# Kernel tuning notes

Measured on AMD Instinct MI355X. Metric: run time of the kernel, lower is better.

Reference implementation:

```python
import jax, jax.numpy as jnp
import numpy as np

N_NODES, N_EDGES, N_FEAT = 50000, 500000, 128
HID, LAT, N_GRAPHS = 256, 64, 512
HEADS, DH = 8, 32  # GAT: 8 heads x 32 = 256
EPS = 1e-5


def _seg_softmax(logits, seg, num):
    m = jax.ops.segment_max(logits, seg, num_segments=num)
    m = jnp.where(jnp.isfinite(m), m, 0.0)
    e = jnp.exp(logits - m[seg])
    s = jax.ops.segment_sum(e, seg, num_segments=num)
    return e / jnp.maximum(s[seg], 1e-16)


def _bn(h, g, b):  # BatchNorm1d, batch statistics
    mu = h.mean(0)
    var = h.var(0)
    return (h - mu) * jax.lax.rsqrt(var + EPS) * g + b


def _ln(h, g, b):
    mu = h.mean(-1, keepdims=True)
    var = h.var(-1, keepdims=True)
    return (h - mu) * jax.lax.rsqrt(var + EPS) * g + b


def setup_inputs() -> dict:
    key = jax.random.key(0)
    ks = iter(jax.random.split(key, 40))
    f = lambda *s: jax.random.normal(next(ks), s, dtype=jnp.float32) * 0.05
    inp = {
        'x': jax.random.normal(next(ks), (N_NODES, N_FEAT), dtype=jnp.float32),
        'W_emb': f(N_FEAT, HID), 'b_emb': f(HID),
        'W_gcn': f(HID, HID), 'b_gcn': f(HID),
        'W_gat': f(HID, HID), 'a_src': f(HEADS, DH), 'a_dst': f(HEADS, DH), 'b_gat': f(HID),
        'W_l': f(HID, HID), 'b_l': f(HID), 'W_r': f(HID, HID),
        'bn_gamma': jnp.ones((3, HID), jnp.float32), 'bn_beta': jnp.zeros((3, HID), jnp.float32),
        'Wg1': f(HID, HID // 2), 'bg1': f(HID // 2), 'Wg2': f(HID // 2, 1), 'bg2': f(1),
        'Wm1': f(HID, HID), 'bm1': f(HID), 'ln_m_g': jnp.ones(HID, jnp.float32), 'ln_m_b': jnp.zeros(HID, jnp.float32),
        'Wm2': f(HID, LAT), 'bm2': f(LAT),
        'Wv1': f(HID, HID), 'bv1': f(HID), 'ln_v_g': jnp.ones(HID, jnp.float32), 'ln_v_b': jnp.zeros(HID, jnp.float32),
        'Wv2': f(HID, LAT), 'bv2': f(LAT),
        'edge_index': jax.random.randint(next(ks), (2, N_EDGES), 0, N_NODES, dtype=jnp.int64),
        'batch': jnp.sort(jax.random.randint(next(ks), (N_NODES,), 0, N_GRAPHS, dtype=jnp.int64)),
    }
    return inp


def _forward(x, W_emb, b_emb, W_gcn, b_gcn, W_gat, a_src, a_dst, b_gat,
             W_l, b_l, W_r, bn_gamma, bn_beta, Wg1, bg1, Wg2, bg2,
             Wm1, bm1, ln_m_g, ln_m_b, Wm2, bm2, Wv1, bv1, ln_v_g, ln_v_b, Wv2, bv2,
             edge_index, batch):
    N = x.shape[0]
    loops = jnp.arange(N)
    src_sl = jnp.concatenate([edge_index[0], loops])  # with self-loops (GCN/GAT)
    dst_sl = jnp.concatenate([edge_index[1], loops])

    h = x @ W_emb + b_emb  # [N, HID]

    # --- layer 0: GCNConv ---
    deg = jax.ops.segment_sum(jnp.ones_like(dst_sl, dtype=h.dtype), dst_sl, num_segments=N)
    dis = jax.lax.rsqrt(deg)
    norm = dis[src_sl] * dis[dst_sl]  # [E+N]
    xt = h @ W_gcn
    out = jax.ops.segment_sum(xt[src_sl] * norm[:, None], dst_sl, num_segments=N) + b_gcn
    out = jax.nn.relu(_bn(out, bn_gamma[0], bn_beta[0]))
    h = h + out

    # --- layer 1: GATConv (8 heads, concat) ---
    xt = (h @ W_gat).reshape(N, HEADS, DH)
    al_src = (xt * a_src).sum(-1)  # [N, H]
    al_dst = (xt * a_dst).sum(-1)
    logits = jax.nn.leaky_relu(al_src[src_sl] + al_dst[dst_sl], 0.2)  # [E+N, H]
    alpha = _seg_softmax(logits, dst_sl, N)
    out = jax.ops.segment_sum(xt[src_sl] * alpha[:, :, None], dst_sl, num_segments=N)
    out = out.reshape(N, HID) + b_gat
    out = jax.nn.relu(_bn(out, bn_gamma[1], bn_beta[1]))
    h = h + out

    # --- layer 2: SAGEConv (mean aggregation, no self-loops) ---
    src, dst = edge_index[0], edge_index[1]
    cnt = jax.ops.segment_sum(jnp.ones_like(dst, dtype=h.dtype), dst, num_segments=N)
    nb_mean = jax.ops.segment_sum(h[src], dst, num_segments=N) / jnp.maximum(cnt, 1.0)[:, None]
    out = nb_mean @ W_l + b_l + h @ W_r
    out = jax.nn.relu(_bn(out, bn_gamma[2], bn_beta[2]))
    h = h + out

    # --- GlobalAttention pooling ---
    gate = (jax.nn.relu(h @ Wg1 + bg1) @ Wg2 + bg2)[:, 0]  # [N]
    w = _seg_softmax(gate, batch, N_GRAPHS)
    h_graph = jax.ops.segment_sum(h * w[:, None], batch, num_segments=N_GRAPHS)  # [G, HID]

    mu = jax.nn.relu(_ln(h_graph @ Wm1 + bm1, ln_m_g, ln_m_b)) @ Wm2 + bm2
    logvar = jax.nn.relu(_ln(h_graph @ Wv1 + bv1, ln_v_g, ln_v_b)) @ Wv2 + bv2
    return mu, logvar


def reference(x, W_emb, b_emb, W_gcn, b_gcn, W_gat, a_src, a_dst, b_gat,
              W_l, b_l, W_r, bn_gamma, bn_beta, Wg1, bg1, Wg2, bg2,
              Wm1, bm1, ln_m_g, ln_m_b, Wm2, bm2, Wv1, bv1, ln_v_g, ln_v_b, Wv2, bv2,
              edge_index, batch):
    return _forward(x, W_emb, b_emb, W_gcn, b_gcn, W_gat, a_src, a_dst, b_gat,
                    W_l, b_l, W_r, bn_gamma, bn_beta, Wg1, bg1, Wg2, bg2,
                    Wm1, bm1, ln_m_g, ln_m_b, Wm2, bm2, Wv1, bv1, ln_v_g, ln_v_b, Wv2, bv2,
                    edge_index, batch)
```

## Files before the change

kernel.cpp:

```cpp
#include <hip/hip_runtime.h>
#include <cstdint>
#include <cstddef>

#define N_NODES 50000
#define N_EDGES 500000
#define NG 512
#define HID 256
#define EPS 1e-5f
#define SCB 49

typedef __attribute__((ext_vector_type(8))) __bf16 bf16x8;
typedef __attribute__((ext_vector_type(8))) ushort u16x8;
typedef __attribute__((ext_vector_type(4))) float f32x4;

__device__ __forceinline__ ushort f2bf(float f) {
  uint32_t u = __float_as_uint(f);
  uint32_t r = (u + 0x7fffu + ((u >> 16) & 1u)) >> 16;
  return (ushort)r;
}
__device__ __forceinline__ float bfu(ushort u) { return __uint_as_float(((uint32_t)u) << 16); }
__device__ __forceinline__ float4 bf4(ushort4 u) {
  return make_float4(bfu(u.x), bfu(u.y), bfu(u.z), bfu(u.w));
}

__global__ void k_csr_count(const int* __restrict__ ei, int* __restrict__ cnt) {
  int e = blockIdx.x * 256 + threadIdx.x;
  if (e < N_EDGES) atomicAdd(&cnt[ei[N_EDGES + e]], 1);
}

__global__ void k_scan_part(const int* __restrict__ cnt, int* __restrict__ psum) {
  __shared__ int red[256];
  int tid = threadIdx.x;
  int i0 = blockIdx.x * 1024 + tid * 4;
  int s = 0;
  if (i0 + 4 <= N_NODES) {
    int4 v = *reinterpret_cast<const int4*>(cnt + i0);
    s = v.x + v.y + v.z + v.w;
  } else {
    for (int k = 0; k < 4; k++)
      if (i0 + k < N_NODES) s += cnt[i0 + k];
  }
  red[tid] = s;
  __syncthreads();
  for (int o = 128; o > 0; o >>= 1) {
    if (tid < o) red[tid] += red[tid + o];
    __syncthreads();
  }
  if (tid == 0) psum[blockIdx.x] = red[0];
}

__global__ void k_scan_top(const int* __restrict__ psum, int* __restrict__ boff,
                           int* __restrict__ row_ptr) {
  int t = threadIdx.x;
  int v = (t < SCB) ? psum[t] : 0;
  int own = v;
  for (int o = 1; o < 64; o <<= 1) {
    int u = __shfl_up(v, o);
    if (t >= o) v += u;
  }
  if (t < SCB) boff[t] = v - own;
  if (t == 63) row_ptr[N_NODES] = v;
}

__global__ void k_scan_out(const int* __restrict__ cnt, const int* __restrict__ boff,
                           int* __restrict__ row_ptr, float* __restrict__ dis) {
  __shared__ int ps[256];
  int tid = threadIdx.x;
  int i0 = blockIdx.x * 1024 + tid * 4;
  int v[4];
#pragma unroll
  for (int k = 0; k < 4; k++) v[k] = (i0 + k < N_NODES) ? cnt[i0 + k] : 0;
  int s = v[0] + v[1] + v[2] + v[3];
  ps[tid] = s;
  __syncthreads();
  for (int o = 1; o < 256; o <<= 1) {
    int add = (tid >= o) ? ps[tid - o] : 0;
    __syncthreads();
    ps[tid] += add;
    __syncthreads();
  }
  int run = boff[blockIdx.x] + ((tid > 0) ? ps[tid - 1] : 0);
#pragma unroll
  for (int k = 0; k < 4; k++) {
    if (i0 + k < N_NODES) {
      row_ptr[i0 + k] = run;
      dis[i0 + k] = rsqrtf((float)v[k] + 1.0f);
      run += v[k];
    }
  }
}

__global__ void k_csr_fill(const int* __restrict__ ei, const int* __restrict__ row_ptr,
                           int* __restrict__ fill, int* __restrict__ col_src) {
  int e = blockIdx.x * 256 + threadIdx.x;
  if (e >= N_EDGES) return;
  int s = ei[e], d = ei[N_EDGES + e];
  int pos = row_ptr[d] + atomicAdd(&fill[d], 1);
  col_src[pos] = s;
}

struct WtArgs {
  const float* src[6];
  ushort* dst[6];
  int K[6];
  int C[6];
  int off[6];
};

__global__ void k_wt_all(WtArgs a) {
  int b = blockIdx.x;
  int ji = 0;
#pragma unroll
  for (int t = 1; t < 6; t++)
    if (b >= a.off[t]) ji = t;
  int K = a.K[ji], C = a.C[ji];
  int i = (b - a.off[ji]) * 256 + threadIdx.x;
  int c = i / K, k = i - c * K;
  a.dst[ji][i] = f2bf(a.src[ji][k * C + c]);
}

__global__ void k_wfold(const float* __restrict__ We, const ushort* __restrict__ Wg_t,
                        ushort* __restrict__ Wc_t, float* __restrict__ bc,
                        const float* __restrict__ b_emb, const float* __restrict__ W_gcn) {
  int c = blockIdx.x;
  int k = threadIdx.x;
  const float* wr = We + k * 256;
  const ushort* gr = Wg_t + c * 256;
  float s = 0.f;
  for (int j = 0; j < 256; j++) s = fmaf(wr[j], bfu(gr[j]), s);
  Wc_t[c * 128 + k] = f2bf(s);
  if (k == 0) {
    float t = 0.f;
    for (int j = 0; j < 256; j++) t = fmaf(b_emb[j], W_gcn[j * 256 + c], t);
    bc[c] = t;
  }
}

template <int K, int C, bool DUAL, bool AFP32, bool GATE, bool GATAL, bool BNF>
__global__ __launch_bounds__(256) void k_mgemm(
    const void* __restrict__ A1v, const ushort* __restrict__ W1t,
    const ushort* __restrict__ A2, const ushort* __restrict__ W2t,
    const float* __restrict__ bias, ushort* __restrict__ out_bf,
    const float* __restrict__ gw, const float* __restrict__ gb,
    float* __restrict__ gate, const float* __restrict__ asv,
    const float* __restrict__ adv, float* __restrict__ als,
    float* __restrict__ ald, const float* __restrict__ scsh,
    ushort* __restrict__ hbuf, int M, int relu) {
  constexpr int KS = K / 32;
  constexpr int KSH = KS / 2;
  constexpr int KHALF = K / 2;
  constexpr int CHKH = KHALF / 8;
  constexpr int NPAN = C / 64;
  constexpr int LOWB = DUAL ? 4 : 2;
  constexpr int NTOT = NPAN * LOWB;
  constexpr int NISS = (64 * CHKH) / 256;
  constexpr int PELEM = 64 * KHALF;
  __shared__ ushort wlds[2 * PELEM];
  const int tid = threadIdx.x;
  const int lane = tid & 63;
  const int wid = tid >> 6;
  const int r16 = lane & 15;
  const int kg = lane >> 4;
  const int rbase = blockIdx.x * 64 + wid * 16;

  const bool avalid = (rbase + r16) < M;
  int arow = rbase + r16;
  if (arow >= M) arow = M - 1;

  bf16x8 af[KS], af2[KS];
  if constexpr (BNF) {
    const ushort* xp = (const ushort*)A1v + (size_t)arow * K + kg * 8;
    ushort* hp = hbuf + (size_t)arow * K + kg * 8;
#pragma unroll
    for (int ks = 0; ks < KS; ks++) {
      int col = kg * 8 + ks * 32;
      u16x8 xv = *reinterpret_cast<const u16x8*>(xp + ks * 32);
      u16x8 hv = *reinterpret_cast<const u16x8*>(hp + ks * 32);
      float4 sc0 = *reinterpret_cast<const float4*>(scsh + col);
      float4 sc1 = *reinterpret_cast<const float4*>(scsh + col + 4);
      float4 sh0 = *reinterpret_cast<const float4*>(scsh + 256 + col);
      float4 sh1 = *reinterpret_cast<const float4*>(scsh + 256 + col + 4);
      float scv[8] = {sc0.x, sc0.y, sc0.z, sc0.w, sc1.x, sc1.y, sc1.z, sc1.w};
      float shv[8] = {sh0.x, sh0.y, sh0.z, sh0.w, sh1.x, sh1.y, sh1.z, sh1.w};
      union { u16x8 u; bf16x8 b; } cv;
#pragma unroll
      for (int j = 0; j < 8; j++) {
        float v = fmaf(bfu(xv[j]), scv[j], shv[j]);
        float hn = bfu(hv[j]) + fmaxf(v, 0.f);
        cv.u[j] = f2bf(hn);
      }
      af[ks] = cv.b;
      if (avalid) *reinterpret_cast<u16x8*>(hp + ks * 32) = cv.u;
    }
  } else if constexpr (AFP32) {
    const float* ap = (const float*)A1v + (size_t)arow * K + kg * 8;
#pragma unroll
    for (int ks = 0; ks < KS; ks++) {
      float4 lo = *reinterpret_cast<const float4*>(ap + ks * 32);
      float4 hi = *reinterpret_cast<const float4*>(ap + ks * 32 + 4);
      union { u16x8 u; bf16x8 b; } cv;
      cv.u = (u16x8){f2bf(lo.x), f2bf(lo.y), f2bf(lo.z), f2bf(lo.w),
                     f2bf(hi.x), f2bf(hi.y), f2bf(hi.z), f2bf(hi.w)};
      af[ks] = cv.b;
    }
  } else {
    const ushort* ap = (const ushort*)A1v + (size_t)arow * K + kg * 8;
#pragma unroll
    for (int ks = 0; ks < KS; ks++)
      af[ks] = *reinterpret_cast<const bf16x8*>(ap + ks * 32);
  }
  if constexpr (DUAL) {
    const ushort* ap = A2 + (size_t)arow * K + kg * 8;
#pragma unroll
    for (int ks = 0; ks < KS; ks++)
      af2[ks] = *reinterpret_cast<const bf16x8*>(ap + ks * 32);
  }

  float greg[4] = {0.f, 0.f, 0.f, 0.f};
  f32x4 acc[4];

#define STAGE_ASYNC(WSRC, PAN, KH, BUF)                                        \
  {                                                                            \
    const ushort* base_ = (WSRC) + (size_t)((PAN) * 64) * K + (KH) * KHALF;    \
    _Pragma("unroll") for (int j = 0; j < NISS; j++) {                         \
      int p_ = j * 256 + tid;                                                  \
      int c_ = p_ / CHKH, jj_ = p_ % CHKH;                                     \
      const ushort* g_ = base_ + c_ * K + (jj_ ^ (c_ & 7)) * 8;                \
      ushort* l_ = &wlds[(BUF) * PELEM + (j * 256 + wid * 64) * 8];            \
      __builtin_amdgcn_global_load_lds(                                        \
          (const __attribute__((address_space(1))) void*)(g_),                 \
          (__attribute__((address_space(3))) void*)(l_), 16, 0, 0);            \
    }                                                                          \
  }

#define COMPUTE(AF, KH, BUF)                                                   \
  {                                                                            \
    const ushort* wb_ = &wlds[(BUF) * PELEM];                                  \
    _Pragma("unroll") for (int ct = 0; ct < 4; ct++) {                         \
      bf16x8 wf[KSH];                                                          \
      int colr = ct * 16 + r16;                                                \
      _Pragma("unroll") for (int ksl = 0; ksl < KSH; ksl++) {                  \
        int slot = colr * CHKH + ((ksl * 4 + kg) ^ (r16 & 7));                 \
        wf[ksl] = *reinterpret_cast<const bf16x8*>(&wb_[slot * 8]);            \
      }                                                                        \
      _Pragma("unroll") for (int ksl = 0; ksl < KSH; ksl++)                    \
        acc[ct] = __builtin_amdgcn_mfma_f32_16x16x32_bf16(                     \
            (AF)[(KH) * KSH + ksl], wf[ksl], acc[ct], 0, 0, 0);                \
    }                                                                          \
  }

  STAGE_ASYNC(W1t, 0, 0, 0);
  __syncthreads();

#pragma unroll
  for (int q = 0; q < NTOT; q++) {
    const int kh = q & 1;
    const int pass = DUAL ? ((q >> 1) & 1) : 0;
    const int pan = DUAL ? (q >> 2) : (q >> 1);
    const int bufq = q & 1;
    const int c0 = pan * 64;
    if ((q & (LOWB - 1)) == 0) {
#pragma unroll
      for (int ct = 0; ct < 4; ct++) acc[ct] = (f32x4){0.f, 0.f, 0.f, 0.f};
    }
    if (q + 1 < NTOT) {
      const int nkh = (q + 1) & 1;
      const int npass = DUAL ? (((q + 1) >> 1) & 1) : 0;
      const int npan = DUAL ? ((q + 1) >> 2) : ((q + 1) >> 1);
      const ushort* Wq = (DUAL && npass) ? W2t : W1t;
      STAGE_ASYNC(Wq, npan, nkh, bufq ^ 1);
    }
    if (DUAL && pass) {
      COMPUTE(af2, kh, bufq);
    } else {
      COMPUTE(af, kh, bufq);
    }
    if ((q & (LOWB - 1)) == (LOWB - 1)) {
      if constexpr (GATE) {
#pragma unroll
        for (int ct = 0; ct < 4; ct++) {
          int col = c0 + ct * 16 + r16;
          float bv = bias[col];
          float wv = gw[col];
#pragma unroll
          for (int i = 0; i < 4; i++) {
            float v = fmaxf(acc[ct][i] + bv, 0.f);
            greg[i] = fmaf(v, wv, greg[i]);
          }
        }
      } else {
#pragma unroll
        for (int ct = 0; ct < 4; ct++) {
          int col = c0 + ct * 16 + r16;
          float bv = bias ? bias[col] : 0.f;
#pragma unroll
          for (int i = 0; i < 4; i++) {
            int row = rbase + kg * 4 + i;
            if (row < M) {
              float v = acc[ct][i] + bv;
              if (relu) v = fmaxf(v, 0.f);
              out_bf[(size_t)row * C + col] = f2bf(v);
            }
          }
        }
      }
      if constexpr (GATAL) {
        float ps_[2][4], pd_[2][4];
#pragma unroll
        for (int h2 = 0; h2 < 2; h2++)
#pragma unroll
          for (int i = 0; i < 4; i++) { ps_[h2][i] = 0.f; pd_[h2][i] = 0.f; }
#pragma unroll
        for (int ct = 0; ct < 4; ct++) {
          int col = c0 + ct * 16 + r16;
          float as_ = asv[col], ad_ = adv[col];
          int h2 = ct >> 1;
#pragma unroll
          for (int i = 0; i < 4; i++) {
            ps_[h2][i] = fmaf(acc[ct][i], as_, ps_[h2][i]);
            pd_[h2][i] = fmaf(acc[ct][i], ad_, pd_[h2][i]);
          }
        }
#pragma unroll
        for (int h2 = 0; h2 < 2; h2++)
#pragma unroll
          for (int i = 0; i < 4; i++) {
#pragma unroll
            for (int o = 1; o < 16; o <<= 1) {
              ps_[h2][i] += __shfl_xor(ps_[h2][i], o);
              pd_[h2][i] += __shfl_xor(pd_[h2][i], o);
            }
          }
        if (r16 == 0) {
#pragma unroll
          for (int i = 0; i < 4; i++) {
            int row = rbase + kg * 4 + i;
            if (row < M) {
              als[row * 8 + pan * 2 + 0] = ps_[0][i];
              ald[row * 8 + pan * 2 + 0] = pd_[0][i];
              als[row * 8 + pan * 2 + 1] = ps_[1][i];
              ald[row * 8 + pan * 2 + 1] = pd_[1][i];
            }
          }
        }
      }
    }
    __syncthreads();
  }

  if constexpr (GATE) {
#pragma unroll
    for (int i = 0; i < 4; i++) {
#pragma unroll
      for (int o = 1; o < 16; o <<= 1) greg[i] += __shfl_xor(greg[i], o);
    }
    if (r16 == 0) {
      float b0 = gb[0];
#pragma unroll
      for (int i = 0; i < 4; i++) {
        int row = rbase + kg * 4 + i;
        if (row < M) gate[row] = greg[i] + b0;
      }
    }
  }
#undef STAGE_ASYNC
#undef COMPUTE
}

__global__ void k_gcn_agg(const ushort* __restrict__ xt, const float* __restrict__ dis,
                          const int* __restrict__ row_ptr, const int* __restrict__ col_src,
                          const float* __restrict__ b_gcn, ushort* __restrict__ outb) {
  int node = blockIdx.x * 4 + (threadIdx.x >> 6);
  if (node >= N_NODES) return;
  int lane = threadIdx.x & 63;
  int half = lane >> 5;
  int c0 = (lane & 31) * 8;
  float di = dis[node];
  float acc[8];
#pragma unroll
  for (int j = 0; j < 8; j++) acc[j] = 0.f;
  int b = row_ptr[node], e = row_ptr[node + 1];
  int g0 = b;
  for (; g0 + 8 <= e; g0 += 8) {
    int i0 = g0 + half * 4;
    int s0 = col_src[i0], s1 = col_src[i0 + 1], s2 = col_src[i0 + 2], s3 = col_src[i0 + 3];
    float w0 = di * dis[s0], w1 = di * dis[s1], w2 = di * dis[s2], w3 = di * dis[s3];
    u16x8 u0 = *reinterpret_cast<const u16x8*>(xt + (size_t)s0 * HID + c0);
    u16x8 u1 = *reinterpret_cast<const u16x8*>(xt + (size_t)s1 * HID + c0);
    u16x8 u2 = *reinterpret_cast<const u16x8*>(xt + (size_t)s2 * HID + c0);
    u16x8 u3 = *reinterpret_cast<const u16x8*>(xt + (size_t)s3 * HID + c0);
#pragma unroll
    for (int j = 0; j < 8; j++) {
      acc[j] = fmaf(bfu(u0[j]), w0, acc[j]);
      acc[j] = fmaf(bfu(u1[j]), w1, acc[j]);
      acc[j] = fmaf(bfu(u2[j]), w2, acc[j]);
      acc[j] = fmaf(bfu(u3[j]), w3, acc[j]);
    }
  }
  for (; g0 + 4 <= e; g0 += 4) {
    int i0 = g0 + half * 2;
    int s0 = col_src[i0], s1 = col_src[i0 + 1];
    float w0 = di * dis[s0], w1 = di * dis[s1];
    u16x8 u0 = *reinterpret_cast<const u16x8*>(xt + (size_t)s0 * HID + c0);
    u16x8 u1 = *reinterpret_cast<const u16x8*>(xt + (size_t)s1 * HID + c0);
#pragma unroll
    for (int j = 0; j < 8; j++) {
      acc[j] = fmaf(bfu(u0[j]), w0, acc[j]);
      acc[j] = fmaf(bfu(u1[j]), w1, acc[j]);
    }
  }
  {
    int i0 = g0 + half * 2;
    int s0 = 0, s1 = 0;
    float w0 = 0.f, w1 = 0.f;
    if (i0 < e) { s0 = col_src[i0]; w0 = di * dis[s0]; }
    if (i0 + 1 < e) { s1 = col_src[i0 + 1]; w1 = di * dis[s1]; }
    u16x8 u0 = *reinterpret_cast<const u16x8*>(xt + (size_t)s0 * HID + c0);
    u16x8 u1 = *reinterpret_cast<const u16x8*>(xt + (size_t)s1 * HID + c0);
#pragma unroll
    for (int j = 0; j < 8; j++) {
      acc[j] = fmaf(bfu(u0[j]), w0, acc[j]);
      acc[j] = fmaf(bfu(u1[j]), w1, acc[j]);
    }
  }
#pragma unroll
  for (int j = 0; j < 8; j++) acc[j] += __shfl_xor(acc[j], 32);
  if (!half) {
    u16x8 un = *reinterpret_cast<const u16x8*>(xt + (size_t)node * HID + c0);
    float w0 = di * di;
    u16x8 r;
#pragma unroll
    for (int j = 0; j < 8; j++) {
      float v = fmaf(bfu(un[j]), w0, acc[j]) + b_gcn[c0 + j];
      r[j] = f2bf(v);
    }
    *reinterpret_cast<u16x8*>(outb + (size_t)node * HID + c0) = r;
  }
}

__device__ __forceinline__ float leaky02(float x) { return x > 0.f ? x : 0.2f * x; }

__global__ void k_gat_agg(const ushort* __restrict__ xt, const float* __restrict__ alsrc,
                          const float* __restrict__ aldst, const int* __restrict__ row_ptr,
                          const int* __restrict__ col_src, const float* __restrict__ b_gat,
                          ushort* __restrict__ outb) {
  int node = blockIdx.x * 4 + (threadIdx.x >> 6);
  if (node >= N_NODES) return;
  int lane = threadIdx.x & 63;
  int half = lane >> 5;
  int l32 = lane & 31;
  int c0 = l32 * 8;
  int hh = l32 >> 2;
  float ad = aldst[node * 8 + hh];
  float acc[8];
#pragma unroll
  for (int j = 0; j < 8; j++) acc[j] = 0.f;
  float s = 0.f;
  int b = row_ptr[node], e = row_ptr[node + 1];
  int g0 = b;
  for (; g0 + 8 <= e; g0 += 8) {
    int i0 = g0 + half * 4;
    int s0 = col_src[i0], s1 = col_src[i0 + 1], s2 = col_src[i0 + 2], s3 = col_src[i0 + 3];
    float g0v = alsrc[s0 * 8 + hh], g1v = alsrc[s1 * 8 + hh];
    float g2v = alsrc[s2 * 8 + hh], g3v = alsrc[s3 * 8 + hh];
    u16x8 u0 = *reinterpret_cast<const u16x8*>(xt + (size_t)s0 * HID + c0);
    u16x8 u1 = *reinterpret_cast<const u16x8*>(xt + (size_t)s1 * HID + c0);
    u16x8 u2 = *reinterpret_cast<const u16x8*>(xt + (size_t)s2 * HID + c0);
    u16x8 u3 = *reinterpret_cast<const u16x8*>(xt + (size_t)s3 * HID + c0);
    float a0 = __expf(leaky02(g0v + ad));
    float a1 = __expf(leaky02(g1v + ad));
    float a2 = __expf(leaky02(g2v + ad));
    float a3 = __expf(leaky02(g3v + ad));
    s += a0 + a1 + a2 + a3;
#pragma unroll
    for (int j = 0; j < 8; j++) {
      acc[j] = fmaf(bfu(u0[j]), a0, acc[j]);
      acc[j] = fmaf(bfu(u1[j]), a1, acc[j]);
      acc[j] = fmaf(bfu(u2[j]), a2, acc[j]);
      acc[j] = fmaf(bfu(u3[j]), a3, acc[j]);
    }
  }
  for (; g0 + 4 <= e; g0 += 4) {
    int i0 = g0 + half * 2;
    int s0 = col_src[i0], s1 = col_src[i0 + 1];
    float a0 = __expf(leaky02(alsrc[s0 * 8 + hh] + ad));
    float a1 = __expf(leaky02(alsrc[s1 * 8 + hh] + ad));
    u16x8 u0 = *reinterpret_cast<const u16x8*>(xt + (size_t)s0 * HID + c0);
    u16x8 u1 = *reinterpret_cast<const u16x8*>(xt + (size_t)s1 * HID + c0);
    s += a0 + a1;
#pragma unroll
    for (int j = 0; j < 8; j++) {
      acc[j] = fmaf(bfu(u0[j]), a0, acc[j]);
      acc[j] = fmaf(bfu(u1[j]), a1, acc[j]);
    }
  }
  {
    int i0 = g0 + half * 2;
    int s0 = 0, s1 = 0;
    float a0 = 0.f, a1 = 0.f;
    if (i0 < e) { s0 = col_src[i0]; a0 = __expf(leaky02(alsrc[s0 * 8 + hh] + ad)); }
    if (i0 + 1 < e) { s1 = col_src[i0 + 1]; a1 = __expf(leaky02(alsrc[s1 * 8 + hh] + ad)); }
    u16x8 u0 = *reinterpret_cast<const u16x8*>(xt + (size_t)s0 * HID + c0);
    u16x8 u1 = *reinterpret_cast<const u16x8*>(xt + (size_t)s1 * HID + c0);
    s += a0 + a1;
#pragma unroll
    for (int j = 0; j < 8; j++) {
      acc[j] = fmaf(bfu(u0[j]), a0, acc[j]);
      acc[j] = fmaf(bfu(u1[j]), a1, acc[j]);
    }
  }
#pragma unroll
  for (int j = 0; j < 8; j++) acc[j] += __shfl_xor(acc[j], 32);
  s += __shfl_xor(s, 32);
  if (!half) {
    float e0 = __expf(leaky02(alsrc[node * 8 + hh] + ad));
    u16x8 un = *reinterpret_cast<const u16x8*>(xt + (size_t)node * HID + c0);
    float inv_s = 1.0f / (s + e0);
    u16x8 r;
#pragma unroll
    for (int j = 0; j < 8; j++) {
      float v = fmaf(bfu(un[j]), e0, acc[j]) * inv_s + b_gat[c0 + j];
      r[j] = f2bf(v);
    }
    *reinterpret_cast<u16x8*>(outb + (size_t)node * HID + c0) = r;
  }
}

__global__ void k_sage_agg(const ushort* __restrict__ h, const int* __restrict__ row_ptr,
                           const int* __restrict__ col_src, ushort* __restrict__ outb) {
  int node = blockIdx.x * 4 + (threadIdx.x >> 6);
  if (node >= N_NODES) return;
  int lane = threadIdx.x & 63;
  int half = lane >> 5;
  int c0 = (lane & 31) * 8;
  float acc[8];
#pragma unroll
  for (int j = 0; j < 8; j++) acc[j] = 0.f;
  int b = row_ptr[node], e = row_ptr[node + 1];
  int g0 = b;
  for (; g0 + 8 <= e; g0 += 8) {
    int i0 = g0 + half * 4;
    int s0 = col_src[i0], s1 = col_src[i0 + 1], s2 = col_src[i0 + 2], s3 = col_src[i0 + 3];
    u16x8 u0 = *reinterpret_cast<const u16x8*>(h + (size_t)s0 * HID + c0);
    u16x8 u1 = *reinterpret_cast<const u16x8*>(h + (size_t)s1 * HID + c0);
    u16x8 u2 = *reinterpret_cast<const u16x8*>(h + (size_t)s2 * HID + c0);
    u16x8 u3 = *reinterpret_cast<const u16x8*>(h + (size_t)s3 * HID + c0);
#pragma unroll
    for (int j = 0; j < 8; j++)
      acc[j] += (bfu(u0[j]) + bfu(u1[j])) + (bfu(u2[j]) + bfu(u3[j]));
  }
  for (; g0 + 4 <= e; g0 += 4) {
    int i0 = g0 + half * 2;
    int s0 = col_src[i0], s1 = col_src[i0 + 1];
    u16x8 u0 = *reinterpret_cast<const u16x8*>(h + (size_t)s0 * HID + c0);
    u16x8 u1 = *reinterpret_cast<const u16x8*>(h + (size_t)s1 * HID + c0);
#pragma unroll
    for (int j = 0; j < 8; j++) acc[j] += bfu(u0[j]) + bfu(u1[j]);
  }
  {
    int i0 = g0 + half * 2;
    int s0 = 0, s1 = 0;
    float w0 = 0.f, w1 = 0.f;
    if (i0 < e) { s0 = col_src[i0]; w0 = 1.f; }
    if (i0 + 1 < e) { s1 = col_src[i0 + 1]; w1 = 1.f; }
    u16x8 u0 = *reinterpret_cast<const u16x8*>(h + (size_t)s0 * HID + c0);
    u16x8 u1 = *reinterpret_cast<const u16x8*>(h + (size_t)s1 * HID + c0);
#pragma unroll
    for (int j = 0; j < 8; j++) {
      acc[j] = fmaf(bfu(u0[j]), w0, acc[j]);
      acc[j] = fmaf(bfu(u1[j]), w1, acc[j]);
    }
  }
#pragma unroll
  for (int j = 0; j < 8; j++) acc[j] += __shfl_xor(acc[j], 32);
  if (!half) {
    float inv = 1.0f / fmaxf((float)(e - b), 1.0f);
    u16x8 r;
#pragma unroll
    for (int j = 0; j < 8; j++) r[j] = f2bf(acc[j] * inv);
    *reinterpret_cast<u16x8*>(outb + (size_t)node * HID + c0) = r;
  }
}

__global__ __launch_bounds__(256) void k_bn_stats(const ushort* __restrict__ x,
                                                  float* __restrict__ stats) {
  int tid = threadIdx.x;
  int cg = tid & 31;
  int rs = tid >> 5;
  int c0 = cg * 8;
  float s[8], q[8];
#pragma unroll
  for (int j = 0; j < 8; j++) { s[j] = 0.f; q[j] = 0.f; }
  for (int r = blockIdx.x * 8 + rs; r < N_NODES; r += gridDim.x * 8) {
    u16x8 v = *reinterpret_cast<const u16x8*>(x + (size_t)r * HID + c0);
#pragma unroll
    for (int j = 0; j < 8; j++) {
      float f = bfu(v[j]);
      s[j] += f;
      q[j] = fmaf(f, f, q[j]);
    }
  }
  __shared__ float ls[512];
  ls[tid] = 0.f;
  ls[tid + 256] = 0.f;
  __syncthreads();
#pragma unroll
  for (int j = 0; j < 8; j++) {
    atomicAdd(&ls[c0 + j], s[j]);
    atomicAdd(&ls[256 + c0 + j], q[j]);
  }
  __syncthreads();
  atomicAdd(&stats[tid], ls[tid]);
  atomicAdd(&stats[tid + 256], ls[tid + 256]);
}

__global__ void k_bn_coef(const float* __restrict__ stats, const float* __restrict__ gamma,
                          const float* __restrict__ beta, float* __restrict__ scsh) {
  int c = threadIdx.x;
  const float invN = 1.0f / (float)N_NODES;
  float mu = stats[c] * invN;
  float var = stats[256 + c] * invN - mu * mu;
  float sc = gamma[c] * rsqrtf(var + EPS);
  scsh[c] = sc;
  scsh[256 + c] = beta[c] - mu * sc;
}

__global__ void k_bn_apply(const ushort* __restrict__ x, const float* __restrict__ scsh,
                           ushort* __restrict__ h_bf) {
  int total = N_NODES * 64;
  for (int i = blockIdx.x * 256 + threadIdx.x; i < total; i += gridDim.x * 256) {
    int c4 = (i & 63) * 4;
    float4 xv = bf4(*reinterpret_cast<const ushort4*>(x + (size_t)i * 4));
    float4 sc = *reinterpret_cast<const float4*>(scsh + c4);
    float4 sh = *reinterpret_cast<const float4*>(scsh + 256 + c4);
    float4 hv = bf4(*reinterpret_cast<const ushort4*>(h_bf + (size_t)i * 4));
    hv.x += fmaxf(fmaf(xv.x, sc.x, sh.x), 0.f);
    hv.y += fmaxf(fmaf(xv.y, sc.y, sh.y), 0.f);
    hv.z += fmaxf(fmaf(xv.z, sc.z, sh.z), 0.f);
    hv.w += fmaxf(fmaf(xv.w, sc.w, sh.w), 0.f);
    *reinterpret_cast<ushort4*>(h_bf + (size_t)i * 4) =
        make_ushort4(f2bf(hv.x), f2bf(hv.y), f2bf(hv.z), f2bf(hv.w));
  }
}

__global__ void k_gstart(const int* __restrict__ batch, int* __restrict__ gstart) {
  int g = blockIdx.x * 256 + threadIdx.x;
  if (g > NG) return;
  int lo = 0, hi = N_NODES;
  while (lo < hi) {
    int mid = (lo + hi) >> 1;
    if (batch[mid] < g) lo = mid + 1; else hi = mid;
  }
  gstart[g] = lo;
}

__global__ void k_pool(const ushort* __restrict__ hb, const float* __restrict__ gate,
                       const int* __restrict__ gstart, float* __restrict__ hg) {
  __shared__ float red[256];
  __shared__ float wbuf[256];
  int g = blockIdx.x, tid = threadIdx.x;
  int b = gstart[g], e = gstart[g + 1];
  float m = -1e30f;
  for (int r = b + tid; r < e; r += 256) m = fmaxf(m, gate[r]);
  red[tid] = m;
  __syncthreads();
  for (int o = 128; o > 0; o >>= 1) {
    if (tid < o) red[tid] = fmaxf(red[tid], red[tid + o]);
    __syncthreads();
  }
  m = red[0];
  __syncthreads();
  float s = 0.f;
  for (int r = b + tid; r < e; r += 256) s += __expf(gate[r] - m);
  red[tid] = s;
  __syncthreads();
  for (int o = 128; o > 0; o >>= 1) {
    if (tid < o) red[tid] += red[tid + o];
    __syncthreads();
  }
  float inv = 1.0f / fmaxf(red[0], 1e-16f);
  __syncthreads();
  float acc = 0.f;
  for (int cb = b; cb < e; cb += 256) {
    int r = cb + tid;
    wbuf[tid] = (r < e) ? __expf(gate[r] - m) : 0.f;
    __syncthreads();
    int n = min(256, e - cb);
    for (int j = 0; j < n; j++)
      acc = fmaf(bfu(hb[(size_t)(cb + j) * HID + tid]), wbuf[j], acc);
    __syncthreads();
  }
  hg[(size_t)g * HID + tid] = acc * inv;
}

__global__ void k_mlp(const float* __restrict__ hg, const float* __restrict__ W1,
                      const float* __restrict__ b1, const float* __restrict__ lng,
                      const float* __restrict__ lnb, const float* __restrict__ W2,
                      const float* __restrict__ b2, float* __restrict__ out) {
  __shared__ float row[HID];
  __shared__ float z[HID];
  __shared__ float red[HID];
  int g = blockIdx.x, tid = threadIdx.x;
  row[tid] = hg[(size_t)g * HID + tid];
  __syncthreads();
  float acc = b1[tid];
  for (int k = 0; k < HID; k++) acc = fmaf(row[k], W1[(size_t)k * HID + tid], acc);
  red[tid] = acc;
  __syncthreads();
  for (int o = 128; o > 0; o >>= 1) {
    if (tid < o) red[tid] += red[tid + o];
    __syncthreads();
  }
  float mu = red[0] * (1.0f / HID);
  __syncthreads();
  red[tid] = acc * acc;
  __syncthreads();
  for (int o = 128; o > 0; o >>= 1) {
    if (tid < o) red[tid] += red[tid + o];
    __syncthreads();
  }
  float var = red[0] * (1.0f / HID) - mu * mu;
  float zz = (acc - mu) * rsqrtf(var + EPS) * lng[tid] + lnb[tid];
  z[tid] = fmaxf(zz, 0.f);
  __syncthreads();
  if (tid < 64) {
    float o = b2[tid];
    for (int k = 0; k < HID; k++) o = fmaf(z[k], W2[(size_t)k * 64 + tid], o);
    out[(size_t)g * 64 + tid] = o;
  }
}

extern "C" void kernel_launch(void* const* d_in, const int* in_sizes, int n_in,
                              void* d_out, int out_size, void* d_ws, size_t ws_size,
                              hipStream_t stream) {
  const float* x     = (const float*)d_in[0];
  const float* W_emb = (const float*)d_in[1];
  const float* b_emb = (const float*)d_in[2];
  const float* W_gcn = (const float*)d_in[3];
  const float* b_gcn = (const float*)d_in[4];
  const float* W_gat = (const float*)d_in[5];
  const float* a_src = (const float*)d_in[6];
  const float* a_dst = (const float*)d_in[7];
  const float* b_gat = (const float*)d_in[8];
  const float* W_l   = (const float*)d_in[9];
  const float* b_l   = (const float*)d_in[10];
  const float* W_r   = (const float*)d_in[11];
  const float* bn_g  = (const float*)d_in[12];
  const float* bn_b  = (const float*)d_in[13];
  const float* Wg1   = (const float*)d_in[14];
  const float* bg1   = (const float*)d_in[15];
  const float* Wg2   = (const float*)d_in[16];
  const float* bg2   = (const float*)d_in[17];
  const float* Wm1   = (const float*)d_in[18];
  const float* bm1   = (const float*)d_in[19];
  const float* lnmg  = (const float*)d_in[20];
  const float* lnmb  = (const float*)d_in[21];
  const float* Wm2   = (const float*)d_in[22];
  const float* bm2   = (const float*)d_in[23];
  const float* Wv1   = (const float*)d_in[24];
  const float* bv1   = (const float*)d_in[25];
  const float* lnvg  = (const float*)d_in[26];
  const float* lnvb  = (const float*)d_in[27];
  const float* Wv2   = (const float*)d_in[28];
  const float* bv2   = (const float*)d_in[29];
  const int* ei      = (const int*)d_in[30];
  const int* batch   = (const int*)d_in[31];
  float* out = (float*)d_out;

  float* ws = (float*)d_ws;
  float* h     = ws;
  float* t1    = h + (size_t)N_NODES * HID;
  float* alsrc = t1 + (size_t)N_NODES * HID;
  float* aldst = alsrc + N_NODES * 8;
  float* dis   = aldst + N_NODES * 8;
  float* gate  = dis + N_NODES;
  float* hg    = gate + N_NODES;
  float* zbase = hg + NG * HID;
  float* bnst  = zbase;
  int* row_cnt = (int*)(zbase + 3 * 512);
  int* fill    = row_cnt + N_NODES;
  int* row_ptr = fill + N_NODES;
  int* col_src = row_ptr + N_NODES + 1;
  int* gstart  = col_src + N_EDGES;
  int* psum    = gstart + NG + 1;
  int* boff    = psum + 64;
  float* scsh  = (float*)(boff + 64);
  float* bc    = scsh + 3 * 512;

  ushort* t1b = (ushort*)t1;

  size_t off = (size_t)((char*)(bc + 256) - (char*)d_ws);
  off = (off + 15) & ~(size_t)15;
  ushort* h_bf   = (ushort*)((char*)d_ws + off);
  ushort* t0_bf  = h_bf + (size_t)N_NODES * HID;
  ushort* wemb_t = t0_bf + (size_t)N_NODES * HID;
  ushort* wgcn_t = wemb_t + 128 * 256;
  ushort* wgat_t = wgcn_t + 256 * 256;
  ushort* wr_t   = wgat_t + 256 * 256;
  ushort* wl_t   = wr_t + 256 * 256;
  ushort* wg1_t  = wl_t + 256 * 256;
  ushort* wc_t   = wg1_t + 256 * 128;

  size_t zbytes = (size_t)3 * 512 * 4 + 2 * (size_t)N_NODES * 4;
  hipMemsetAsync(zbase, 0, zbytes, stream);

  k_csr_count<<<(N_EDGES + 255) / 256, 256, 0, stream>>>(ei, row_cnt);
  k_scan_part<<<SCB, 256, 0, stream>>>(row_cnt, psum);
  k_scan_top<<<1, 64, 0, stream>>>(psum, boff, row_ptr);
  k_scan_out<<<SCB, 256, 0, stream>>>(row_cnt, boff, row_ptr, dis);
  k_csr_fill<<<(N_EDGES + 255) / 256, 256, 0, stream>>>(ei, row_ptr, fill, col_src);

  WtArgs wa;
  wa.src[0] = W_emb; wa.dst[0] = wemb_t; wa.K[0] = 128; wa.C[0] = 256; wa.off[0] = 0;
  wa.src[1] = W_gcn; wa.dst[1] = wgcn_t; wa.K[1] = 256; wa.C[1] = 256; wa.off[1] = 128;
  wa.src[2] = W_gat; wa.dst[2] = wgat_t; wa.K[2] = 256; wa.C[2] = 256; wa.off[2] = 384;
  wa.src[3] = W_r;   wa.dst[3] = wr_t;   wa.K[3] = 256; wa.C[3] = 256; wa.off[3] = 640;
  wa.src[4] = W_l;   wa.dst[4] = wl_t;   wa.K[4] = 256; wa.C[4] = 256; wa.off[4] = 896;
  wa.src[5] = Wg1;   wa.dst[5] = wg1_t;  wa.K[5] = 256; wa.C[5] = 128; wa.off[5] = 1152;
  k_wt_all<<<1280, 256, 0, stream>>>(wa);

  k_wfold<<<256, 128, 0, stream>>>(W_emb, wgcn_t, wc_t, bc, b_emb, W_gcn);

  const int RB = (N_NODES + 63) / 64;
  const int AB = (N_NODES + 3) / 4;

  k_mgemm<128, 256, false, true, false, false, false><<<RB, 256, 0, stream>>>(
      x, wemb_t, nullptr, nullptr, b_emb, h_bf, nullptr, nullptr, nullptr,
      nullptr, nullptr, nullptr, nullptr, nullptr, nullptr, N_NODES, 0);

  k_mgemm<128, 256, false, true, false, false, false><<<RB, 256, 0, stream>>>(
      x, wc_t, nullptr, nullptr, bc, t0_bf, nullptr, nullptr, nullptr,
      nullptr, nullptr, nullptr, nullptr, nullptr, nullptr, N_NODES, 0);
  k_gcn_agg<<<AB, 256, 0, stream>>>(t0_bf, dis, row_ptr, col_src, b_gcn, t1b);
  k_bn_stats<<<1024, 256, 0, stream>>>(t1b, bnst);
  k_bn_coef<<<1, 256, 0, stream>>>(bnst, bn_g, bn_b, scsh);

  k_mgemm<256, 256, false, false, false, true, true><<<RB, 256, 0, stream>>>(
      t1b, wgat_t, nullptr, nullptr, nullptr, t0_bf, nullptr, nullptr, nullptr,
      a_src, a_dst, alsrc, aldst, scsh, h_bf, N_NODES, 0);
  k_gat_agg<<<AB, 256, 0, stream>>>(t0_bf, alsrc, aldst, row_ptr, col_src, b_gat, t1b);
  k_bn_stats<<<1024, 256, 0, stream>>>(t1b, bnst + 512);
  k_bn_coef<<<1, 256, 0, stream>>>(bnst + 512, bn_g + HID, bn_b + HID, scsh + 512);
  k_bn_apply<<<1024, 256, 0, stream>>>(t1b, scsh + 512, h_bf);

  k_sage_agg<<<AB, 256, 0, stream>>>(h_bf, row_ptr, col_src, t0_bf);
  k_mgemm<256, 256, true, false, false, false, false><<<RB, 256, 0, stream>>>(
      h_bf, wr_t, t0_bf, wl_t, b_l, t1b, nullptr, nullptr, nullptr,
      nullptr, nullptr, nullptr, nullptr, nullptr, nullptr, N_NODES, 0);
  k_bn_stats<<<1024, 256, 0, stream>>>(t1b, bnst + 1024);
  k_bn_coef<<<1, 256, 0, stream>>>(bnst + 1024, bn_g + 2 * HID, bn_b + 2 * HID, scsh + 1024);

  k_mgemm<256, 128, false, false, true, false, true><<<RB, 256, 0, stream>>>(
      t1b, wg1_t, nullptr, nullptr, bg1, nullptr, Wg2, bg2, gate,
      nullptr, nullptr, nullptr, nullptr, scsh + 1024, h_bf, N_NODES, 1);
  k_gstart<<<3, 256, 0, stream>>>(batch, gstart);
  k_pool<<<NG, 256, 0, stream>>>(h_bf, gate, gstart, hg);

  k_mlp<<<NG, 256, 0, stream>>>(hg, Wm1, bm1, lnmg, lnmb, Wm2, bm2, out);
  k_mlp<<<NG, 256, 0, stream>>>(hg, Wv1, bv1, lnvg, lnvb, Wv2, bv2, out + (size_t)NG * 64);
}
```

Before: 564.3 us.

## Split GEMM output columns across grid Y and drop folded-weight GEMM

```diff
diff --git a/kernel.cpp b/kernel.cpp
--- a/kernel.cpp
+++ b/kernel.cpp
@@ -119,24 +119,7 @@
   a.dst[ji][i] = f2bf(a.src[ji][k * C + c]);
 }
 
-__global__ void k_wfold(const float* __restrict__ We, const ushort* __restrict__ Wg_t,
-                        ushort* __restrict__ Wc_t, float* __restrict__ bc,
-                        const float* __restrict__ b_emb, const float* __restrict__ W_gcn) {
-  int c = blockIdx.x;
-  int k = threadIdx.x;
-  const float* wr = We + k * 256;
-  const ushort* gr = Wg_t + c * 256;
-  float s = 0.f;
-  for (int j = 0; j < 256; j++) s = fmaf(wr[j], bfu(gr[j]), s);
-  Wc_t[c * 128 + k] = f2bf(s);
-  if (k == 0) {
-    float t = 0.f;
-    for (int j = 0; j < 256; j++) t = fmaf(b_emb[j], W_gcn[j * 256 + c], t);
-    bc[c] = t;
-  }
-}
-
-template <int K, int C, bool DUAL, bool AFP32, bool GATE, bool GATAL, bool BNF>
+template <int K, int C, int CSPLIT, bool DUAL, bool AFP32, bool GATE, bool GATAL, bool BNF>
 __global__ __launch_bounds__(256) void k_mgemm(
     const void* __restrict__ A1v, const ushort* __restrict__ W1t,
     const ushort* __restrict__ A2, const ushort* __restrict__ W2t,
@@ -145,14 +128,15 @@
     float* __restrict__ gate, const float* __restrict__ asv,
     const float* __restrict__ adv, float* __restrict__ als,
     float* __restrict__ ald, const float* __restrict__ scsh,
-    ushort* __restrict__ hbuf, int M, int relu) {
+    const ushort* __restrict__ hbin, ushort* __restrict__ hbout, int M, int relu) {
   constexpr int KS = K / 32;
   constexpr int KSH = KS / 2;
   constexpr int KHALF = K / 2;
   constexpr int CHKH = KHALF / 8;
   constexpr int NPAN = C / 64;
+  constexpr int NPANL = NPAN / CSPLIT;
   constexpr int LOWB = DUAL ? 4 : 2;
-  constexpr int NTOT = NPAN * LOWB;
+  constexpr int NTOT = NPANL * LOWB;
   constexpr int NISS = (64 * CHKH) / 256;
   constexpr int PELEM = 64 * KHALF;
   __shared__ ushort wlds[2 * PELEM];
@@ -162,6 +146,7 @@
   const int r16 = lane & 15;
   const int kg = lane >> 4;
   const int rbase = blockIdx.x * 64 + wid * 16;
+  const int pbase = blockIdx.y * NPANL;
 
   const bool avalid = (rbase + r16) < M;
   int arow = rbase + r16;
@@ -170,7 +155,8 @@
   bf16x8 af[KS], af2[KS];
   if constexpr (BNF) {
     const ushort* xp = (const ushort*)A1v + (size_t)arow * K + kg * 8;
-    ushort* hp = hbuf + (size_t)arow * K + kg * 8;
+    const ushort* hp = hbin + (size_t)arow * K + kg * 8;
+    ushort* hq = hbout + (size_t)arow * K + kg * 8;
 #pragma unroll
     for (int ks = 0; ks < KS; ks++) {
       int col = kg * 8 + ks * 32;
@@ -190,7 +176,7 @@
         cv.u[j] = f2bf(hn);
       }
       af[ks] = cv.b;
-      if (avalid) *reinterpret_cast<u16x8*>(hp + ks * 32) = cv.u;
+      if (avalid && blockIdx.y == 0) *reinterpret_cast<u16x8*>(hq + ks * 32) = cv.u;
     }
   } else if constexpr (AFP32) {
     const float* ap = (const float*)A1v + (size_t)arow * K + kg * 8;
@@ -249,14 +235,14 @@
     }                                                                          \
   }
 
-  STAGE_ASYNC(W1t, 0, 0, 0);
+  STAGE_ASYNC(W1t, pbase, 0, 0);
   __syncthreads();
 
 #pragma unroll
   for (int q = 0; q < NTOT; q++) {
     const int kh = q & 1;
     const int pass = DUAL ? ((q >> 1) & 1) : 0;
-    const int pan = DUAL ? (q >> 2) : (q >> 1);
+    const int pan = pbase + (DUAL ? (q >> 2) : (q >> 1));
     const int bufq = q & 1;
     const int c0 = pan * 64;
     if ((q & (LOWB - 1)) == 0) {
@@ -266,7 +252,7 @@
     if (q + 1 < NTOT) {
       const int nkh = (q + 1) & 1;
       const int npass = DUAL ? (((q + 1) >> 1) & 1) : 0;
-      const int npan = DUAL ? ((q + 1) >> 2) : ((q + 1) >> 1);
+      const int npan = pbase + (DUAL ? ((q + 1) >> 2) : ((q + 1) >> 1));
       const ushort* Wq = (DUAL && npass) ? W2t : W1t;
       STAGE_ASYNC(Wq, npan, nkh, bufq ^ 1);
     }
@@ -355,11 +341,11 @@
       for (int o = 1; o < 16; o <<= 1) greg[i] += __shfl_xor(greg[i], o);
     }
     if (r16 == 0) {
-      float b0 = gb[0];
+      float b0 = (blockIdx.y == 0) ? gb[0] : 0.f;
 #pragma unroll
       for (int i = 0; i < 4; i++) {
         int row = rbase + kg * 4 + i;
-        if (row < M) gate[row] = greg[i] + b0;
+        if (row < M) atomicAdd(&gate[row], greg[i] + b0);
       }
     }
   }
@@ -785,11 +771,11 @@
   int* psum    = gstart + NG + 1;
   int* boff    = psum + 64;
   float* scsh  = (float*)(boff + 64);
-  float* bc    = scsh + 3 * 512;
 
   ushort* t1b = (ushort*)t1;
-
-  size_t off = (size_t)((char*)(bc + 256) - (char*)d_ws);
+  ushort* hB  = (ushort*)h;
+
+  size_t off = (size_t)((char*)(scsh + 3 * 512) - (char*)d_ws);
   off = (off + 15) & ~(size_t)15;
   ushort* h_bf   = (ushort*)((char*)d_ws + off);
   ushort* t0_bf  = h_bf + (size_t)N_NODES * HID;
@@ -799,7 +785,6 @@
   ushort* wr_t   = wgat_t + 256 * 256;
   ushort* wl_t   = wr_t + 256 * 256;
   ushort* wg1_t  = wl_t + 256 * 256;
-  ushort* wc_t   = wg1_t + 256 * 128;
 
   size_t zbytes = (size_t)3 * 512 * 4 + 2 * (size_t)N_NODES * 4;
   hipMemsetAsync(zbase, 0, zbytes, stream);
@@ -819,40 +804,39 @@
   wa.src[5] = Wg1;   wa.dst[5] = wg1_t;  wa.K[5] = 256; wa.C[5] = 128; wa.off[5] = 1152;
   k_wt_all<<<1280, 256, 0, stream>>>(wa);
 
-  k_wfold<<<256, 128, 0, stream>>>(W_emb, wgcn_t, wc_t, bc, b_emb, W_gcn);
-
   const int RB = (N_NODES + 63) / 64;
   const int AB = (N_NODES + 3) / 4;
 
-  k_mgemm<128, 256, false, true, false, false, false><<<RB, 256, 0, stream>>>(
+  k_mgemm<128, 256, 1, false, true, false, false, false><<<dim3(RB, 1), 256, 0, stream>>>(
       x, wemb_t, nullptr, nullptr, b_emb, h_bf, nullptr, nullptr, nullptr,
-      nullptr, nullptr, nullptr, nullptr, nullptr, nullptr, N_NODES, 0);
-
-  k_mgemm<128, 256, false, true, false, false, false><<<RB, 256, 0, stream>>>(
-      x, wc_t, nullptr, nullptr, bc, t0_bf, nullptr, nullptr, nullptr,
-      nullptr, nullptr, nullptr, nullptr, nullptr, nullptr, N_NODES, 0);
+      nullptr, nullptr, nullptr, nullptr, nullptr, nullptr, nullptr, N_NODES, 0);
+
+  k_mgemm<256, 256, 2, false, false, false, false, false><<<dim3(RB, 2), 256, 0, stream>>>(
+      h_bf, wgcn_t, nullptr, nullptr, nullptr, t0_bf, nullptr, nullptr, nullptr,
+      nullptr, nullptr, nullptr, nullptr, nullptr, nullptr, nullptr, N_NODES, 0);
   k_gcn_agg<<<AB, 256, 0, stream>>>(t0_bf, dis, row_ptr, col_src, b_gcn, t1b);
   k_bn_stats<<<1024, 256, 0, stream>>>(t1b, bnst);
   k_bn_coef<<<1, 256, 0, stream>>>(bnst, bn_g, bn_b, scsh);
 
-  k_mgemm<256, 256, false, false, false, true, true><<<RB, 256, 0, stream>>>(
+  k_mgemm<256, 256, 2, false, false, false, true, true><<<dim3(RB, 2), 256, 0, stream>>>(
       t1b, wgat_t, nullptr, nullptr, nullptr, t0_bf, nullptr, nullptr, nullptr,
-      a_src, a_dst, alsrc, aldst, scsh, h_bf, N_NODES, 0);
+      a_src, a_dst, alsrc, aldst, scsh, h_bf, hB, N_NODES, 0);
   k_gat_agg<<<AB, 256, 0, stream>>>(t0_bf, alsrc, aldst, row_ptr, col_src, b_gat, t1b);
   k_bn_stats<<<1024, 256, 0, stream>>>(t1b, bnst + 512);
   k_bn_coef<<<1, 256, 0, stream>>>(bnst + 512, bn_g + HID, bn_b + HID, scsh + 512);
-  k_bn_apply<<<1024, 256, 0, stream>>>(t1b, scsh + 512, h_bf);
-
-  k_sage_agg<<<AB, 256, 0, stream>>>(h_bf, row_ptr, col_src, t0_bf);
-  k_mgemm<256, 256, true, false, false, false, false><<<RB, 256, 0, stream>>>(
-      h_bf, wr_t, t0_bf, wl_t, b_l, t1b, nullptr, nullptr, nullptr,
-      nullptr, nullptr, nullptr, nullptr, nullptr, nullptr, N_NODES, 0);
+  k_bn_apply<<<1024, 256, 0, stream>>>(t1b, scsh + 512, hB);
+
+  k_sage_agg<<<AB, 256, 0, stream>>>(hB, row_ptr, col_src, t0_bf);
+  k_mgemm<256, 256, 2, true, false, false, false, false><<<dim3(RB, 2), 256, 0, stream>>>(
+      hB, wr_t, t0_bf, wl_t, b_l, t1b, nullptr, nullptr, nullptr,
+      nullptr, nullptr, nullptr, nullptr, nullptr, nullptr, nullptr, N_NODES, 0);
   k_bn_stats<<<1024, 256, 0, stream>>>(t1b, bnst + 1024);
   k_bn_coef<<<1, 256, 0, stream>>>(bnst + 1024, bn_g + 2 * HID, bn_b + 2 * HID, scsh + 1024);
 
-  k_mgemm<256, 128, false, false, true, false, true><<<RB, 256, 0, stream>>>(
+  hipMemsetAsync(gate, 0, (size_t)N_NODES * 4, stream);
+  k_mgemm<256, 128, 2, false, false, true, false, true><<<dim3(RB, 2), 256, 0, stream>>>(
       t1b, wg1_t, nullptr, nullptr, bg1, nullptr, Wg2, bg2, gate,
-      nullptr, nullptr, nullptr, nullptr, scsh + 1024, h_bf, N_NODES, 1);
+      nullptr, nullptr, nullptr, nullptr, scsh + 1024, hB, h_bf, N_NODES, 1);
   k_gstart<<<3, 256, 0, stream>>>(batch, gstart);
   k_pool<<<NG, 256, 0, stream>>>(h_bf, gate, gstart, hg);
 
```

Result: no change. 556.4 us (-1.4%).
